# Optimization experiments

Measured on AMD Instinct MI355X. Metric: run time of the kernel, lower is better.

## Reference

```python
import jax, jax.numpy as jnp
import numpy as np

B, N, C, H = 4, 1024, 1024, 16
D = C // H  # head_dim = 64


def setup_inputs() -> dict:
    key = jax.random.key(0)
    k1, k2, k3 = jax.random.split(key, 3)
    x = jax.random.normal(k1, (B, N, C), dtype=jnp.float32)
    Wqkv = jax.random.normal(k2, (3 * C, C), dtype=jnp.float32) * (C ** -0.5)
    Wproj = jax.random.normal(k3, (C, C), dtype=jnp.float32) * (C ** -0.5)
    bproj = jnp.zeros((C,), dtype=jnp.float32)
    epoch = 25  # selects mask_2 (window w=8) per the original branching
    return {"x": x, "Wqkv": Wqkv, "Wproj": Wproj, "bproj": bproj, "epoch": epoch}


def _band_mask(n, w):
    # get_attn_mask(N, w) == (|i - j| <= w) for every row (boundary cases included)
    idx = jnp.arange(n)
    return jnp.abs(idx[:, None] - idx[None, :]) <= w


def reference(x, Wqkv, Wproj, bproj, epoch):
    b, n, c = x.shape
    d = c // H
    # qkv linear (no bias), then the module's per-head interleaved split:
    # view(B,N,H,3d) -> permute(B,H,N,3d) -> tensor_split into q,k,v
    qkv = jnp.einsum('bnc,oc->bno', x, Wqkv)            # [B,N,3C]
    qkv = qkv.reshape(b, n, H, 3 * d).transpose(0, 2, 1, 3)  # [B,H,N,3d]
    q, k, v = jnp.split(qkv, 3, axis=-1)                # each [B,H,N,d]
    scale = d ** -0.5
    score = jnp.einsum('bhid,bhjd->bhij', q, k) * scale  # [B,H,N,N]
    if epoch is not None and epoch < 50:
        if epoch < 20:
            w = 6
        elif epoch < 30:
            w = 8
        elif epoch < 40:
            w = 10
        else:
            w = 12
        mask = _band_mask(n, w)  # [N,N] bool
        score = jnp.where(mask[None, None], score, jnp.float32(-1e9))
    attn = jax.nn.softmax(score, axis=-1)
    ctx = jnp.einsum('bhij,bhjd->bhid', attn, v)         # [B,H,N,d]
    ctx = ctx.transpose(0, 2, 1, 3).reshape(b, n, c)     # [B,N,C]
    out = jnp.einsum('bnc,oc->bno', ctx, Wproj) + bproj
    return out
```

## Files before the change

### kernel.cpp

```cpp
#include <hip/hip_runtime.h>
#include <hip/hip_bf16.h>


typedef __bf16 bf16x8_t __attribute__((ext_vector_type(8)));
typedef unsigned short u16x8_t __attribute__((ext_vector_type(8)));
typedef float f32x4_t __attribute__((ext_vector_type(4)));

__device__ __forceinline__ void load_lds16(const void* g, void* l) {
    __builtin_amdgcn_global_load_lds(
        (__attribute__((address_space(1))) void*)(g),
        (__attribute__((address_space(3))) void*)(l),
        16, 0, 0);
}

__device__ __forceinline__ u16x8_t cvt8(float4 u, float4 v) {
    union { u16x8_t p; __hip_bfloat16 h[8]; } w;
    w.h[0] = __float2bfloat16(u.x); w.h[1] = __float2bfloat16(u.y);
    w.h[2] = __float2bfloat16(u.z); w.h[3] = __float2bfloat16(u.w);
    w.h[4] = __float2bfloat16(v.x); w.h[5] = __float2bfloat16(v.y);
    w.h[6] = __float2bfloat16(v.z); w.h[7] = __float2bfloat16(v.w);
    return w.p;
}

__global__ __launch_bounds__(256) void convert_xw(
    const float* __restrict__ x, const float* __restrict__ wqkv,
    __hip_bfloat16* __restrict__ xb, __hip_bfloat16* __restrict__ wqkvb)
{
    const size_t t = (size_t)blockIdx.x * 256 + threadIdx.x;
    size_t i = t * 8;
    const float* src;
    __hip_bfloat16* dst;
    if (i < 4194304) {
        src = x; dst = xb;
    } else {
        src = wqkv; dst = wqkvb; i -= 4194304;
    }
    float4 v0 = *reinterpret_cast<const float4*>(src + i);
    float4 v1 = *reinterpret_cast<const float4*>(src + i + 4);
    *reinterpret_cast<u16x8_t*>(dst + i) = cvt8(v0, v1);
}

__global__ __launch_bounds__(512, 2) void gemm1_qkv256(
    const __hip_bfloat16* __restrict__ A,
    const __hip_bfloat16* __restrict__ B,
    __hip_bfloat16* __restrict__ C)
{
    __shared__ __align__(16) char smem[114688];
    const int tid = threadIdx.x;

    const int orig = blockIdx.y * 16 + blockIdx.x;
    const int xcd = orig & 7, slot = orig >> 3;
    const int hi = slot >> 4;
    const int s  = xcd * 2 + hi;
    const int w  = slot & 15;
    const int m0 = ((s & 3) * 4 + (w & 3)) * 256;
    const int n0 = ((s >> 2) * 4 + (w >> 2)) * 192;

    const int wave = tid >> 6, lane = tid & 63;
    const int wr = wave >> 2, wc = wave & 3;
    const int lr = lane & 15, kg = lane >> 4;
    const int K = 1024, Nn = 3072;

    const int qa0 = tid, qa1 = tid + 512;
    const int qb0 = tid, qb1 = tid + 256;
    const int ra0 = qa0 >> 2, sa0 = ((qa0 & 3) ^ ((ra0 >> 1) & 3)) * 16;
    const int ra1 = qa1 >> 2, sa1 = ((qa1 & 3) ^ ((ra1 >> 1) & 3)) * 16;
    const int rb0 = qb0 >> 2, sb0 = ((qb0 & 3) ^ ((rb0 >> 1) & 3)) * 16;
    const int rb1 = qb1 >> 2, sb1 = ((qb1 & 3) ^ ((rb1 >> 1) & 3)) * 16;
    const char* Asrc0 = (const char*)(A + (size_t)(m0 + ra0) * K) + sa0;
    const char* Asrc1 = (const char*)(A + (size_t)(m0 + ra1) * K) + sa1;
    const char* Bsrc0 = (const char*)(B + (size_t)(n0 + rb0) * K) + sb0;
    const char* Bsrc1 = (const char*)(B + (size_t)(n0 + rb1) * K) + sb1;
    const bool bextra = (tid >= 256);

#define STAGE_A(t) { const int sb_ = ((t) & 3) * 28672; const int ko_ = (t) * 64; \
    load_lds16(Asrc0 + ko_, smem + sb_ + qa0 * 16);                                \
    load_lds16(Asrc1 + ko_, smem + sb_ + qa1 * 16); }
#define STAGE_B(t) { const int sb_ = ((t) & 3) * 28672; const int ko_ = (t) * 64; \
    load_lds16(Bsrc0 + ko_, smem + sb_ + 16384 + qb0 * 16);                        \
    if (bextra) load_lds16(Bsrc1 + ko_, smem + sb_ + 16384 + qb1 * 16); }

    f32x4_t acc[8][3] = {};
    const int rsw = ((kg ^ ((lr >> 1) & 3)) * 16);
    const int arow = wr * 128 + lr;
    const int brow = wc * 48 + lr;

    STAGE_A(0); STAGE_B(0);
    STAGE_A(1); STAGE_B(1);
    if (!bextra) { asm volatile("s_waitcnt vmcnt(3)" ::: "memory"); }
    else         { asm volatile("s_waitcnt vmcnt(4)" ::: "memory"); }
    __builtin_amdgcn_s_barrier();

    for (int t = 0; t < 32; ++t) {
        const int sb_ = (t & 3) * 28672;
        bf16x8_t a_[8], b_[3];
#pragma unroll
        for (int mi = 0; mi < 4; ++mi)
            a_[mi] = *(const bf16x8_t*)(smem + sb_ + (arow + mi * 16) * 64 + rsw);
#pragma unroll
        for (int ni = 0; ni < 3; ++ni)
            b_[ni] = *(const bf16x8_t*)(smem + sb_ + 16384 + (brow + ni * 16) * 64 + rsw);
        if (t < 30) STAGE_A(t + 2);
        __builtin_amdgcn_s_barrier();
        __builtin_amdgcn_s_setprio(1);
#pragma unroll
        for (int mi = 0; mi < 4; ++mi)
#pragma unroll
            for (int ni = 0; ni < 3; ++ni)
                acc[mi][ni] = __builtin_amdgcn_mfma_f32_16x16x32_bf16(
                    a_[mi], b_[ni], acc[mi][ni], 0, 0, 0);
        __builtin_amdgcn_s_setprio(0);
        __builtin_amdgcn_s_barrier();
#pragma unroll
        for (int mi = 4; mi < 8; ++mi)
            a_[mi] = *(const bf16x8_t*)(smem + sb_ + (arow + mi * 16) * 64 + rsw);
        if (t < 30) {
            STAGE_B(t + 2);
            if (!bextra) { asm volatile("s_waitcnt vmcnt(3)" ::: "memory"); }
            else         { asm volatile("s_waitcnt vmcnt(4)" ::: "memory"); }
        } else {
            asm volatile("s_waitcnt vmcnt(0)" ::: "memory");
        }
        __builtin_amdgcn_s_barrier();
        __builtin_amdgcn_s_setprio(1);
#pragma unroll
        for (int mi = 4; mi < 8; ++mi)
#pragma unroll
            for (int ni = 0; ni < 3; ++ni)
                acc[mi][ni] = __builtin_amdgcn_mfma_f32_16x16x32_bf16(
                    a_[mi], b_[ni], acc[mi][ni], 0, 0, 0);
        __builtin_amdgcn_s_setprio(0);
        __builtin_amdgcn_s_barrier();
    }
#undef STAGE_A
#undef STAGE_B

    __syncthreads();
    __hip_bfloat16* cl = (__hip_bfloat16*)smem;
#pragma unroll
    for (int mi = 0; mi < 8; ++mi)
#pragma unroll
        for (int ni = 0; ni < 3; ++ni)
#pragma unroll
            for (int r = 0; r < 4; ++r)
                cl[(wr * 128 + mi * 16 + kg * 4 + r) * 200 + wc * 48 + ni * 16 + lr] =
                    __float2bfloat16(acc[mi][ni][r]);
    __syncthreads();
#pragma unroll
    for (int c = 0; c < 12; ++c) {
        const int id = tid + c * 512;
        const int row = id / 24, cc = id - row * 24;
        f32x4_t v = *(const f32x4_t*)(smem + row * 400 + cc * 16);
        *(f32x4_t*)((char*)C + ((size_t)(m0 + row) * Nn + n0) * 2 + cc * 16) = v;
    }
}

__global__ __launch_bounds__(512, 2) void gemm2_proj(
    const __hip_bfloat16* __restrict__ A,
    const float* __restrict__ B,
    float* __restrict__ C,
    const float* __restrict__ bias)
{
    __shared__ __align__(16) char smem[65536];
    const int tid = threadIdx.x;
    const int orig = blockIdx.y * 8 + blockIdx.x;
    const int wgid = (orig & 7) * 32 + (orig >> 3);
    const int m0 = (wgid >> 3) * 128, n0 = (wgid & 7) * 128;

    const int wave = tid >> 6, lane = tid & 63;
    const int wr = wave >> 2, wc = wave & 3;
    const int lr = lane & 15, kg = lane >> 4;
    const int K = 1024, Nn = 1024;

    const int q = tid;
    const int row = q >> 2, cw = ((q & 3) ^ ((row >> 1) & 3)) * 8;
    const __hip_bfloat16* Ap = A + (size_t)(m0 + row) * K + cw;
    const float*          Bp = B + (size_t)(n0 + row) * K + cw;

    float4 av = {}, bv0 = {}, bv1 = {};

#define LOADR2(t) { const int ko_ = (t) * 32;                                  \
    av  = *(const float4*)(Ap + ko_);                        \
    bv0 = *(const float4*)(Bp + ko_); bv1 = *(const float4*)(Bp + ko_ + 4); }
#define WRITE2(t) { char* d_ = smem + ((t) & 3) * 16384;                       \
    *(float4*)(d_ + q * 16) = av;                                              \
    *(u16x8_t*)(d_ + 8192 + q * 16) = cvt8(bv0, bv1); }

    f32x4_t acc[4][2] = {};
    const int rsw = ((kg ^ ((lr >> 1) & 3)) * 16);
    const int arow = wr * 64 + lr;
    const int brow = wc * 32 + lr;

    LOADR2(0); WRITE2(0);
    LOADR2(1); WRITE2(1);
    LOADR2(2);
    __syncthreads();

    for (int t = 0; t < 32; ++t) {
        const int sb_ = (t & 3) * 16384;
        bf16x8_t a_[4], b_[2];
#pragma unroll
        for (int mi = 0; mi < 4; ++mi)
            a_[mi] = *(const bf16x8_t*)(smem + sb_ + (arow + mi * 16) * 64 + rsw);
#pragma unroll
        for (int ni = 0; ni < 2; ++ni)
            b_[ni] = *(const bf16x8_t*)(smem + sb_ + 8192 + (brow + ni * 16) * 64 + rsw);
        if (t < 30) WRITE2(t + 2);
        if (t < 29) LOADR2(t + 3);
        __builtin_amdgcn_s_setprio(1);
#pragma unroll
        for (int mi = 0; mi < 4; ++mi)
#pragma unroll
            for (int ni = 0; ni < 2; ++ni)
                acc[mi][ni] = __builtin_amdgcn_mfma_f32_16x16x32_bf16(
                    a_[mi], b_[ni], acc[mi][ni], 0, 0, 0);
        __builtin_amdgcn_s_setprio(0);
        __syncthreads();
    }
#undef LOADR2
#undef WRITE2

    float* cf = (float*)smem;
#pragma unroll
    for (int p = 0; p < 2; ++p) {
        if (p) __syncthreads();
        if (wr == p) {
#pragma unroll
            for (int mi = 0; mi < 4; ++mi)
#pragma unroll
                for (int ni = 0; ni < 2; ++ni) {
                    const int scol = wc * 32 + ni * 16 + lr;
#pragma unroll
                    for (int r = 0; r < 4; ++r)
                        cf[(mi * 16 + kg * 4 + r) * 132 + scol] = acc[mi][ni][r];
                }
        }
        __syncthreads();
#pragma unroll
        for (int cc = 0; cc < 4; ++cc) {
            const int chunk = tid + cc * 512;
            const int srow = chunk >> 5;
            const int sc = (chunk & 31) * 4;
            f32x4_t v = *(const f32x4_t*)(smem + srow * 528 + sc * 4);
            const f32x4_t bv = *(const f32x4_t*)(bias + n0 + sc);
            v += bv;
            *(f32x4_t*)(C + (size_t)(m0 + p * 64 + srow) * Nn + n0 + sc) = v;
        }
    }
}

__global__ __launch_bounds__(256) void attn_band_mfma(
    const __hip_bfloat16* __restrict__ qkv,
    __hip_bfloat16* __restrict__ ctx,
    const int* __restrict__ epoch_ptr)
{
    __shared__ __align__(16) __hip_bfloat16 K_lds[128 * 64];
    __shared__ __align__(16) __hip_bfloat16 V_lds[64 * 136];
    __shared__ __hip_bfloat16 P_lds[4][16 * 40];

    const int tid = threadIdx.x;
    const int wave = tid >> 6, lane = tid & 63;
    const int lr = lane & 15, kg = lane >> 4;

    const int bid = blockIdx.x;
    const int tg = bid & 15;
    const int bh = bid >> 4;
    const int h = bh & 15, b = bh >> 4;
    const int base = tg * 64;
    const int i0 = base + wave * 16;

    const int e = *epoch_ptr;
    int w;
    if      (e < 20) w = 6;
    else if (e < 30) w = 8;
    else if (e < 40) w = 10;
    else if (e < 50) w = 12;
    else             w = 1023;

    const size_t rowb = (size_t)b * 1024;
    const int hq = h * 192;

#pragma unroll
    for (int it = 0; it < 4; ++it) {
        const int q = tid + it * 256;
        const int row = q >> 3, s = q & 7;
        const int c = s ^ (row & 7);
        int gk = base - 32 + row;
        gk = gk < 0 ? 0 : (gk > 1023 ? 1023 : gk);
        load_lds16(qkv + (rowb + gk) * 3072 + hq + 64 + c * 8,
                   (char*)K_lds + q * 16);
    }
    {
        const int pr = tid & 63, dg = tid >> 6;
        int gk0 = base - 32 + 2 * pr, gk1 = gk0 + 1;
        gk0 = gk0 < 0 ? 0 : (gk0 > 1023 ? 1023 : gk0);
        gk1 = gk1 < 0 ? 0 : (gk1 > 1023 ? 1023 : gk1);
        const __hip_bfloat16* v0 = qkv + (rowb + gk0) * 3072 + hq + 128 + dg * 16;
        const __hip_bfloat16* v1 = qkv + (rowb + gk1) * 3072 + hq + 128 + dg * 16;
        u16x8_t a0 = *(const u16x8_t*)v0, b0 = *(const u16x8_t*)(v0 + 8);
        u16x8_t a1 = *(const u16x8_t*)v1, b1 = *(const u16x8_t*)(v1 + 8);
#pragma unroll
        for (int c2 = 0; c2 < 8; ++c2) {
            *(unsigned int*)&V_lds[(dg * 16 + c2) * 136 + 2 * pr] =
                (unsigned int)a0[c2] | ((unsigned int)a1[c2] << 16);
            *(unsigned int*)&V_lds[(dg * 16 + 8 + c2) * 136 + 2 * pr] =
                (unsigned int)b0[c2] | ((unsigned int)b1[c2] << 16);
        }
    }

    bf16x8_t aq[2];
#pragma unroll
    for (int ks = 0; ks < 2; ++ks)
        aq[ks] = *(const bf16x8_t*)(qkv + (rowb + i0 + lr) * 3072 + hq + ks * 32 + kg * 8);

    __syncthreads();

    float m[4] = {-1e30f, -1e30f, -1e30f, -1e30f};
    float l[4] = {0.f, 0.f, 0.f, 0.f};
    f32x4_t o[4] = {};

    int jlo = i0 - w;      if (jlo < 0) jlo = 0;
    int jhi = i0 + 15 + w; if (jhi > 1023) jhi = 1023;
    const int t0 = (base >> 5) - 1;

    for (int p = (jlo >> 5); p <= (jhi >> 5); ++p) {
        const int kb = p * 32;
        const int tl = p - t0;

        f32x4_t s2[2] = {};
#pragma unroll
        for (int t = 0; t < 2; ++t)
#pragma unroll
            for (int ks = 0; ks < 2; ++ks) {
                const int lkr = tl * 32 + t * 16 + lr;
                bf16x8_t bk = *(const bf16x8_t*)(
                    (char*)K_lds + lkr * 128 + (((ks * 4 + kg) ^ (lr & 7)) * 16));
                s2[t] = __builtin_amdgcn_mfma_f32_16x16x32_bf16(aq[ks], bk, s2[t], 0, 0, 0);
            }

        float sv[2][4];
#pragma unroll
        for (int t = 0; t < 2; ++t)
#pragma unroll
            for (int r = 0; r < 4; ++r) {
                const int qi = i0 + kg * 4 + r;
                const int j  = kb + t * 16 + lr;
                int d = qi - j; if (d < 0) d = -d;
                sv[t][r] = (d <= w) ? s2[t][r] * 0.125f : -1e30f;
            }

        float tm[4];
#pragma unroll
        for (int r = 0; r < 4; ++r) tm[r] = fmaxf(sv[0][r], sv[1][r]);
#pragma unroll
        for (int msk = 1; msk < 16; msk <<= 1)
#pragma unroll
            for (int r = 0; r < 4; ++r) tm[r] = fmaxf(tm[r], __shfl_xor(tm[r], msk));

        float sc[4], ps[4], pvv[2][4];
#pragma unroll
        for (int r = 0; r < 4; ++r) {
            const float mn = fmaxf(m[r], tm[r]);
            sc[r] = __expf(m[r] - mn);
            pvv[0][r] = __expf(sv[0][r] - mn);
            pvv[1][r] = __expf(sv[1][r] - mn);
            ps[r] = pvv[0][r] + pvv[1][r];
            m[r] = mn;
        }
#pragma unroll
        for (int msk = 1; msk < 16; msk <<= 1)
#pragma unroll
            for (int r = 0; r < 4; ++r) ps[r] += __shfl_xor(ps[r], msk);
#pragma unroll
        for (int r = 0; r < 4; ++r) l[r] = l[r] * sc[r] + ps[r];
#pragma unroll
        for (int ni = 0; ni < 4; ++ni)
#pragma unroll
            for (int r = 0; r < 4; ++r) o[ni][r] *= sc[r];

#pragma unroll
        for (int t = 0; t < 2; ++t)
#pragma unroll
            for (int r = 0; r < 4; ++r)
                P_lds[wave][(kg * 4 + r) * 40 + t * 16 + lr] =
                    __float2bfloat16(pvv[t][r]);

        bf16x8_t ap = *(const bf16x8_t*)&P_lds[wave][lr * 40 + kg * 8];
#pragma unroll
        for (int ni = 0; ni < 4; ++ni) {
            bf16x8_t bv = *(const bf16x8_t*)&V_lds[(ni * 16 + lr) * 136 + tl * 32 + kg * 8];
            o[ni] = __builtin_amdgcn_mfma_f32_16x16x32_bf16(ap, bv, o[ni], 0, 0, 0);
        }
    }

#pragma unroll
    for (int ni = 0; ni < 4; ++ni)
#pragma unroll
        for (int r = 0; r < 4; ++r)
            ctx[(rowb + i0 + kg * 4 + r) * 1024 + h * 64 + ni * 16 + lr] =
                __float2bfloat16(o[ni][r] / l[r]);
}

extern "C" void kernel_launch(void* const* d_in, const int* in_sizes, int n_in,
                              void* d_out, int out_size, void* d_ws, size_t ws_size,
                              hipStream_t stream)
{
    const float* x     = (const float*)d_in[0];
    const float* Wqkv  = (const float*)d_in[1];
    const float* Wproj = (const float*)d_in[2];
    const float* bproj = (const float*)d_in[3];
    const int*   epoch = (const int*)d_in[4];

    char* ws = (char*)d_ws;
    __hip_bfloat16* xb    = (__hip_bfloat16*)(ws);
    __hip_bfloat16* wqkvb = (__hip_bfloat16*)(ws + 8388608);
    __hip_bfloat16* qkvb  = (__hip_bfloat16*)(ws + 16777216);
    __hip_bfloat16* ctxb  = (__hip_bfloat16*)(ws + 16777216 + 25165824);

    convert_xw<<<3584, 256, 0, stream>>>(x, Wqkv, xb, wqkvb);

    gemm1_qkv256<<<dim3(16, 16), 512, 0, stream>>>(xb, wqkvb, qkvb);

    attn_band_mfma<<<1024, 256, 0, stream>>>(qkvb, ctxb, epoch);

    gemm2_proj<<<dim3(8, 32), 512, 0, stream>>>(
        ctxb, Wproj, (float*)d_out, bproj);
}
```

Before: 71.55 us.

## Restructure QKV GEMM to 256x256 tiles with 8-phase quadrant pipeline

Replaces the 256x192 QKV GEMM with a 256x256 tile using a K-step of 128. LDS is split into double-buffered A/B halves, and each iteration runs eight phases, one per 128x128 quadrant. Each phase interleaves a direct-to-LDS load of a future half-tile with MFMA work on the current one, and the grid shrinks to 192 workgroups with XCD-aware remapping. It aims for higher arithmetic intensity and finer-grained overlap of global loads with compute. The cost is 128KB of LDS and fewer workgroups than CUs, which may leave some units idle.

New measurement: 73.94 us. 3.3% more time.

```diff
diff --git a/kernel.cpp b/kernel.cpp
--- a/kernel.cpp
+++ b/kernel.cpp
@@ -40,118 +40,112 @@
     *reinterpret_cast<u16x8_t*>(dst + i) = cvt8(v0, v1);
 }
 
-__global__ __launch_bounds__(512, 2) void gemm1_qkv256(
+__global__ __launch_bounds__(512, 2) void gemm1_qkv8(
     const __hip_bfloat16* __restrict__ A,
     const __hip_bfloat16* __restrict__ B,
     __hip_bfloat16* __restrict__ C)
 {
-    __shared__ __align__(16) char smem[114688];
+    __shared__ __align__(16) char smem[131072];
     const int tid = threadIdx.x;
-
-    const int orig = blockIdx.y * 16 + blockIdx.x;
-    const int xcd = orig & 7, slot = orig >> 3;
-    const int hi = slot >> 4;
-    const int s  = xcd * 2 + hi;
-    const int w  = slot & 15;
-    const int m0 = ((s & 3) * 4 + (w & 3)) * 256;
-    const int n0 = ((s >> 2) * 4 + (w >> 2)) * 192;
+    const int orig = blockIdx.y * 12 + blockIdx.x;
+    const int wgid = (orig & 7) * 24 + (orig >> 3);
+    const int m0 = (wgid / 12) * 256, n0 = (wgid % 12) * 256;
 
     const int wave = tid >> 6, lane = tid & 63;
     const int wr = wave >> 2, wc = wave & 3;
     const int lr = lane & 15, kg = lane >> 4;
-    const int K = 1024, Nn = 3072;
-
-    const int qa0 = tid, qa1 = tid + 512;
-    const int qb0 = tid, qb1 = tid + 256;
-    const int ra0 = qa0 >> 2, sa0 = ((qa0 & 3) ^ ((ra0 >> 1) & 3)) * 16;
-    const int ra1 = qa1 >> 2, sa1 = ((qa1 & 3) ^ ((ra1 >> 1) & 3)) * 16;
-    const int rb0 = qb0 >> 2, sb0 = ((qb0 & 3) ^ ((rb0 >> 1) & 3)) * 16;
-    const int rb1 = qb1 >> 2, sb1 = ((qb1 & 3) ^ ((rb1 >> 1) & 3)) * 16;
-    const char* Asrc0 = (const char*)(A + (size_t)(m0 + ra0) * K) + sa0;
-    const char* Asrc1 = (const char*)(A + (size_t)(m0 + ra1) * K) + sa1;
-    const char* Bsrc0 = (const char*)(B + (size_t)(n0 + rb0) * K) + sb0;
-    const char* Bsrc1 = (const char*)(B + (size_t)(n0 + rb1) * K) + sb1;
-    const bool bextra = (tid >= 256);
-
-#define STAGE_A(t) { const int sb_ = ((t) & 3) * 28672; const int ko_ = (t) * 64; \
-    load_lds16(Asrc0 + ko_, smem + sb_ + qa0 * 16);                                \
-    load_lds16(Asrc1 + ko_, smem + sb_ + qa1 * 16); }
-#define STAGE_B(t) { const int sb_ = ((t) & 3) * 28672; const int ko_ = (t) * 64; \
-    load_lds16(Bsrc0 + ko_, smem + sb_ + 16384 + qb0 * 16);                        \
-    if (bextra) load_lds16(Bsrc1 + ko_, smem + sb_ + 16384 + qb1 * 16); }
-
-    f32x4_t acc[8][3] = {};
-    const int rsw = ((kg ^ ((lr >> 1) & 3)) * 16);
-    const int arow = wr * 128 + lr;
-    const int brow = wc * 48 + lr;
-
-    STAGE_A(0); STAGE_B(0);
-    STAGE_A(1); STAGE_B(1);
-    if (!bextra) { asm volatile("s_waitcnt vmcnt(3)" ::: "memory"); }
-    else         { asm volatile("s_waitcnt vmcnt(4)" ::: "memory"); }
-    __builtin_amdgcn_s_barrier();
-
-    for (int t = 0; t < 32; ++t) {
-        const int sb_ = (t & 3) * 28672;
-        bf16x8_t a_[8], b_[3];
-#pragma unroll
-        for (int mi = 0; mi < 4; ++mi)
-            a_[mi] = *(const bf16x8_t*)(smem + sb_ + (arow + mi * 16) * 64 + rsw);
-#pragma unroll
-        for (int ni = 0; ni < 3; ++ni)
-            b_[ni] = *(const bf16x8_t*)(smem + sb_ + 16384 + (brow + ni * 16) * 64 + rsw);
-        if (t < 30) STAGE_A(t + 2);
-        __builtin_amdgcn_s_barrier();
-        __builtin_amdgcn_s_setprio(1);
-#pragma unroll
-        for (int mi = 0; mi < 4; ++mi)
-#pragma unroll
-            for (int ni = 0; ni < 3; ++ni)
-                acc[mi][ni] = __builtin_amdgcn_mfma_f32_16x16x32_bf16(
-                    a_[mi], b_[ni], acc[mi][ni], 0, 0, 0);
-        __builtin_amdgcn_s_setprio(0);
-        __builtin_amdgcn_s_barrier();
-#pragma unroll
-        for (int mi = 4; mi < 8; ++mi)
-            a_[mi] = *(const bf16x8_t*)(smem + sb_ + (arow + mi * 16) * 64 + rsw);
-        if (t < 30) {
-            STAGE_B(t + 2);
-            if (!bextra) { asm volatile("s_waitcnt vmcnt(3)" ::: "memory"); }
-            else         { asm volatile("s_waitcnt vmcnt(4)" ::: "memory"); }
-        } else {
-            asm volatile("s_waitcnt vmcnt(0)" ::: "memory");
-        }
-        __builtin_amdgcn_s_barrier();
-        __builtin_amdgcn_s_setprio(1);
-#pragma unroll
-        for (int mi = 4; mi < 8; ++mi)
-#pragma unroll
-            for (int ni = 0; ni < 3; ++ni)
-                acc[mi][ni] = __builtin_amdgcn_mfma_f32_16x16x32_bf16(
-                    a_[mi], b_[ni], acc[mi][ni], 0, 0, 0);
-        __builtin_amdgcn_s_setprio(0);
-        __builtin_amdgcn_s_barrier();
-    }
+
+    const int rr = tid >> 3;
+    const int cch = (tid & 7) ^ (rr & 7);
+    const __hip_bfloat16* ApSrc0 = A + (size_t)(m0 + rr) * 1024 + cch * 8;
+    const __hip_bfloat16* ApSrc1 = A + (size_t)(m0 + 128 + rr) * 1024 + cch * 8;
+    const __hip_bfloat16* BpSrc0 = B + (size_t)(n0 + (rr >> 5) * 64 + (rr & 31)) * 1024 + cch * 8;
+    const __hip_bfloat16* BpSrc1 = B + (size_t)(n0 + 128 + (rr >> 5) * 64 + (rr & 31)) * 1024 + cch * 8;
+
+#define STAGE_A(D, MH, KT) if ((KT) < 16) {                                     \
+    const size_t o_ = (size_t)(MH) * 65536 + (size_t)(KT) * 64;                 \
+    load_lds16(ApSrc0 + o_, smem + (D) * 65536 + (MH) * 16384 + tid * 16);      \
+    load_lds16(ApSrc1 + o_, smem + (D) * 65536 + (MH) * 16384 + (tid + 512) * 16); }
+#define STAGE_B(D, NH, KT) if ((KT) < 16) {                                     \
+    const size_t o_ = (size_t)(NH) * 32768 + (size_t)(KT) * 64;                 \
+    load_lds16(BpSrc0 + o_, smem + (D) * 65536 + 32768 + (NH) * 16384 + tid * 16); \
+    load_lds16(BpSrc1 + o_, smem + (D) * 65536 + 32768 + (NH) * 16384 + (tid + 512) * 16); }
+
+    f32x4_t acc[8][4] = {};
+    const int aBase = (wr * 64 + lr) * 128;
+    const int bBase = (wc * 32 + lr) * 128;
+    const int ch0 = ((kg) ^ (lr & 7)) * 16;
+    const int ch1 = ((4 + kg) ^ (lr & 7)) * 16;
+
+#define VMW(N) asm volatile("s_waitcnt vmcnt(" #N ")" ::: "memory")
+
+#define PH(D, MH, NH, STMT) {                                                   \
+    __builtin_amdgcn_s_barrier();                                               \
+    bf16x8_t aF[4][2], bF[2][2];                                                \
+    _Pragma("unroll") for (int mi2 = 0; mi2 < 4; ++mi2) {                       \
+        const int rb_ = (D) * 65536 + (MH) * 16384 + aBase + mi2 * 2048;        \
+        aF[mi2][0] = *(const bf16x8_t*)(smem + rb_ + ch0);                      \
+        aF[mi2][1] = *(const bf16x8_t*)(smem + rb_ + ch1); }                    \
+    _Pragma("unroll") for (int ni2 = 0; ni2 < 2; ++ni2) {                       \
+        const int rb_ = (D) * 65536 + 32768 + (NH) * 16384 + bBase + ni2 * 2048;\
+        bF[ni2][0] = *(const bf16x8_t*)(smem + rb_ + ch0);                      \
+        bF[ni2][1] = *(const bf16x8_t*)(smem + rb_ + ch1); }                    \
+    STMT;                                                                       \
+    __builtin_amdgcn_s_setprio(1);                                              \
+    _Pragma("unroll") for (int ks = 0; ks < 2; ++ks)                            \
+    _Pragma("unroll") for (int mi2 = 0; mi2 < 4; ++mi2)                         \
+    _Pragma("unroll") for (int ni2 = 0; ni2 < 2; ++ni2)                         \
+        acc[(MH) * 4 + mi2][(NH) * 2 + ni2] =                                   \
+            __builtin_amdgcn_mfma_f32_16x16x32_bf16(                            \
+                aF[mi2][ks], bF[ni2][ks], acc[(MH) * 4 + mi2][(NH) * 2 + ni2],  \
+                0, 0, 0);                                                       \
+    __builtin_amdgcn_s_setprio(0); }
+
+    STAGE_A(0, 0, 0); STAGE_B(0, 0, 0);
+    STAGE_A(0, 1, 0); STAGE_B(0, 1, 0);
+    STAGE_A(1, 0, 1); STAGE_B(1, 0, 1);
+
+    for (int it = 0; it < 8; ++it) {
+        const int k0 = 2 * it;
+        VMW(8); PH(0, 0, 0, STAGE_A(1, 1, k0 + 1));
+        VMW(6); PH(0, 0, 1, STAGE_B(1, 1, k0 + 1));
+                PH(0, 1, 0, STAGE_A(0, 0, k0 + 2));
+                PH(0, 1, 1, STAGE_B(0, 0, k0 + 2));
+        VMW(8); PH(1, 0, 0, STAGE_A(0, 1, k0 + 2));
+        VMW(6); PH(1, 0, 1, STAGE_B(0, 1, k0 + 2));
+                PH(1, 1, 0, STAGE_A(1, 0, k0 + 3));
+                PH(1, 1, 1, STAGE_B(1, 0, k0 + 3));
+    }
+#undef PH
+#undef VMW
 #undef STAGE_A
 #undef STAGE_B
 
     __syncthreads();
     __hip_bfloat16* cl = (__hip_bfloat16*)smem;
 #pragma unroll
-    for (int mi = 0; mi < 8; ++mi)
-#pragma unroll
-        for (int ni = 0; ni < 3; ++ni)
-#pragma unroll
-            for (int r = 0; r < 4; ++r)
-                cl[(wr * 128 + mi * 16 + kg * 4 + r) * 200 + wc * 48 + ni * 16 + lr] =
-                    __float2bfloat16(acc[mi][ni][r]);
-    __syncthreads();
-#pragma unroll
-    for (int c = 0; c < 12; ++c) {
-        const int id = tid + c * 512;
-        const int row = id / 24, cc = id - row * 24;
-        f32x4_t v = *(const f32x4_t*)(smem + row * 400 + cc * 16);
-        *(f32x4_t*)((char*)C + ((size_t)(m0 + row) * Nn + n0) * 2 + cc * 16) = v;
+    for (int p = 0; p < 2; ++p) {
+        if (p) __syncthreads();
+        if (wr == p) {
+#pragma unroll
+            for (int mi = 0; mi < 8; ++mi)
+#pragma unroll
+                for (int ni = 0; ni < 4; ++ni)
+#pragma unroll
+                    for (int r = 0; r < 4; ++r)
+                        cl[((mi >> 2) * 64 + (mi & 3) * 16 + kg * 4 + r) * 264 +
+                           wc * 64 + (ni >> 1) * 32 + (ni & 1) * 16 + lr] =
+                            __float2bfloat16(acc[mi][ni][r]);
+        }
+        __syncthreads();
+#pragma unroll
+        for (int c = 0; c < 8; ++c) {
+            const int ch = tid + c * 512;
+            const int row = ch >> 5, cc = ch & 31;
+            f32x4_t v = *(const f32x4_t*)(smem + row * 528 + cc * 16);
+            *(f32x4_t*)((char*)C + ((size_t)(m0 + p * 128 + row) * 3072 + n0) * 2 +
+                        cc * 16) = v;
+        }
     }
 }
 
@@ -180,7 +174,7 @@
     float4 av = {}, bv0 = {}, bv1 = {};
 
 #define LOADR2(t) { const int ko_ = (t) * 32;                                  \
-    av  = *(const float4*)(Ap + ko_);                        \
+    av  = *(const float4*)(Ap + ko_);                                          \
     bv0 = *(const float4*)(Bp + ko_); bv1 = *(const float4*)(Bp + ko_ + 4); }
 #define WRITE2(t) { char* d_ = smem + ((t) & 3) * 16384;                       \
     *(float4*)(d_ + q * 16) = av;                                              \
@@ -419,7 +413,7 @@
 
     convert_xw<<<3584, 256, 0, stream>>>(x, Wqkv, xb, wqkvb);
 
-    gemm1_qkv256<<<dim3(16, 16), 512, 0, stream>>>(xb, wqkvb, qkvb);
+    gemm1_qkv8<<<dim3(12, 16), 512, 0, stream>>>(xb, wqkvb, qkvb);
 
     attn_band_mfma<<<1024, 256, 0, stream>>>(qkvb, ctxb, epoch);
 
```
